# Kernel tuning notes

Hardware: AMD Instinct MI355X
Metric: run time of the kernel (lower is better)

Reference implementation:

```python
import jax, jax.numpy as jnp
import numpy as np

BLOCK_SIZE = 8
SELECT_TOPK = 32
HIDDEN = 512
CHANNELS = 384
NUM_HEADS = 8
B, H, W = 8, 64, 64


def setup_inputs() -> dict:
    key = jax.random.key(0)
    ks = jax.random.split(key, 8)
    num_block_tot = (H // BLOCK_SIZE) * (W // BLOCK_SIZE)
    bs2 = BLOCK_SIZE * BLOCK_SIZE
    x = jax.random.normal(ks[0], (B, H, W, CHANNELS), dtype=jnp.float32)
    aw = jax.random.normal(ks[1], (NUM_HEADS, B, num_block_tot, bs2, bs2 + SELECT_TOPK), dtype=jnp.float32)
    attn_weights = jax.nn.softmax(aw, axis=-1)  # module expects sum(-1)==1
    weights = jax.random.uniform(ks[2], (B, num_block_tot, SELECT_TOPK), dtype=jnp.float32)
    indexes = jax.random.randint(ks[3], (B, num_block_tot, SELECT_TOPK), 0, H * W)
    in_proj_w = jax.random.normal(ks[4], (3 * HIDDEN, CHANNELS), dtype=jnp.float32) * 0.02
    in_proj_b = jax.random.normal(ks[5], (3 * HIDDEN,), dtype=jnp.float32) * 0.02
    out_proj_w = jax.random.normal(ks[6], (CHANNELS, HIDDEN), dtype=jnp.float32) * 0.02
    out_proj_b = jax.random.normal(ks[7], (CHANNELS,), dtype=jnp.float32) * 0.02
    return {"x": x, "attn_weights": attn_weights, "weights": weights,
            "in_proj_w": in_proj_w, "in_proj_b": in_proj_b,
            "out_proj_w": out_proj_w, "out_proj_b": out_proj_b,
            "indexes": indexes}


def reference(x, attn_weights, weights, in_proj_w, in_proj_b, out_proj_w, out_proj_b, indexes):
    batch, height, width, _ = x.shape
    bsz = BLOCK_SIZE
    nbh, nbw = height // bsz, width // bsz
    nbt = nbh * nbw
    num_heads = attn_weights.shape[0]
    hid = HIDDEN
    hd = hid // num_heads
    topk = SELECT_TOPK

    proj = jnp.einsum('bhwc,oc->bhwo', x, in_proj_w) + in_proj_b  # (B,H,W,3*hid)
    s, xh, y = jnp.split(proj, 3, axis=-1)
    xh = xh * jnp.tanh(s)  # Balancer/Whiten/Identity are identity in fwd

    # top-k gathered tokens: (B, nbt, topk, hid) without (B,nbt,num_tokens,hid) blowup
    x_flat = xh.reshape(batch, height * width, hid)
    sel = jax.vmap(lambda xf, ix: xf[ix])(x_flat, indexes)  # (B,nbt,topk,hid)
    sel = sel * weights[..., None]
    sel = sel.reshape(batch, nbt, topk, num_heads, hd).transpose(3, 0, 1, 2, 4)  # (nh,B,nbt,topk,hd)

    # block-local tokens: (nh, B, nbt, bsz^2, hd)
    blk = xh.reshape(batch, nbh, bsz, nbw, bsz, num_heads, hd)
    blk = blk.transpose(5, 0, 1, 3, 2, 4, 6).reshape(num_heads, batch, nbt, bsz * bsz, hd)

    kv = jnp.concatenate([blk, sel], axis=3)  # (nh,B,nbt,bsz^2+topk,hd)
    out = jnp.einsum('hbnqk,hbnkd->hbnqd', attn_weights, kv)  # (nh,B,nbt,bsz^2,hd)

    out = out.reshape(num_heads, batch, nbh, nbw, bsz, bsz, hd)
    out = out.transpose(1, 2, 4, 3, 5, 0, 6).reshape(batch, height, width, hid)
    out = out * y
    return jnp.einsum('bhwd,cd->bhwc', out, out_proj_w) + out_proj_b
```

## Files before the change

### kernel.cpp

```cpp
#include <hip/hip_runtime.h>
#include <hip/hip_bf16.h>
#include <stdint.h>

#define CH   384
#define HID  512
#define NHD  8
#define MTOT 32768

typedef __attribute__((ext_vector_type(8))) short bf16x8;
typedef __attribute__((ext_vector_type(4))) float f32x4;
typedef unsigned short u16;

__device__ __forceinline__ float bf2f(u16 v){ return __uint_as_float(((unsigned)v)<<16); }
__device__ __forceinline__ u16 f2bf(float f){
  unsigned u = __float_as_uint(f);
  return (u16)((u + 0x7fffu + ((u>>16)&1u)) >> 16);
}
__device__ __forceinline__ void gload_lds16(const void* g, void* l){
  __builtin_amdgcn_global_load_lds((const __attribute__((address_space(1))) void*)g,
                                   (__attribute__((address_space(3))) void*)l, 16, 0, 0);
}

__global__ void k_cvt(const float* __restrict__ in, u16* __restrict__ out, int n4){
  int i = blockIdx.x*blockDim.x + threadIdx.x;
  int stride = gridDim.x*blockDim.x;
  for (; i < n4; i += stride){
    float4 v = ((const float4*)in)[i];
    ushort4 o; o.x=f2bf(v.x); o.y=f2bf(v.y); o.z=f2bf(v.z); o.w=f2bf(v.w);
    ((ushort4*)out)[i] = o;
  }
}

__global__ void k_gemm1(const u16* __restrict__ xb, const u16* __restrict__ w1b,
                        const float* __restrict__ b1,
                        u16* __restrict__ xh, u16* __restrict__ yb)
{
  __shared__ short lA[128*64];
  __shared__ short lB[96*64];
  const int tid = threadIdx.x;
  const int w = tid >> 6, lw = tid & 63;
  const int m0 = blockIdx.x * 128;
  const int h0 = blockIdx.y * 32;

  f32x4 acc[2][6] = {};

  for (int kt = 0; kt < CH/64; ++kt){
    const int kbase = kt*64;
    #pragma unroll
    for (int i = 0; i < 4; ++i){
      int chunk = i*4 + w;
      int row = chunk*8 + (lw>>3);
      int sl  = (lw&7) ^ (row&7);
      gload_lds16(xb + (size_t)(m0+row)*CH + kbase + sl*8, &lA[chunk*512]);
    }
    #pragma unroll
    for (int i = 0; i < 3; ++i){
      int chunk = i*4 + w;
      int row = chunk*8 + (lw>>3);
      int grow = (row>>5)*HID + h0 + (row&31);
      int sl = (lw&7) ^ (row&7);
      gload_lds16(w1b + (size_t)grow*CH + kbase + sl*8, &lB[chunk*512]);
    }
    __syncthreads();
    #pragma unroll
    for (int ks = 0; ks < 2; ++ks){
      bf16x8 af[2], bfr[6];
      #pragma unroll
      for (int mi=0; mi<2; ++mi){
        int row = w*32 + mi*16 + (lw&15);
        int sl = (ks*4 + (lw>>4)) ^ (row&7);
        af[mi] = *(const bf16x8*)&lA[row*64 + sl*8];
      }
      #pragma unroll
      for (int nj=0; nj<6; ++nj){
        int row = nj*16 + (lw&15);
        int sl = (ks*4 + (lw>>4)) ^ (row&7);
        bfr[nj] = *(const bf16x8*)&lB[row*64 + sl*8];
      }
      #pragma unroll
      for (int mi=0; mi<2; ++mi)
        #pragma unroll
        for (int nj=0; nj<6; ++nj)
          acc[mi][nj] = __builtin_amdgcn_mfma_f32_16x16x32_bf16(af[mi], bfr[nj], acc[mi][nj], 0,0,0);
    }
    __syncthreads();
  }

  const int lc = lw & 15, lr4 = (lw>>4)*4;
  #pragma unroll
  for (int f=0; f<2; ++f){
    int col = h0 + f*16 + lc;
    float bs = b1[col], bx = b1[512+col], by = b1[1024+col];
    #pragma unroll
    for (int mi=0; mi<2; ++mi){
      #pragma unroll
      for (int j=0; j<4; ++j){
        int row = m0 + w*32 + mi*16 + lr4 + j;
        float s  = acc[mi][0+f][j] + bs;
        float xv = (acc[mi][2+f][j] + bx) * tanhf(s);
        float yv = acc[mi][4+f][j] + by;
        xh[(size_t)row*HID + col] = f2bf(xv);
        yb[(size_t)row*HID + col] = f2bf(yv);
      }
    }
  }
}

__global__ void k_attn(const float* __restrict__ aw, const float* __restrict__ wts,
                       const int* __restrict__ idxs,
                       const u16* __restrict__ xh, const u16* __restrict__ yb,
                       u16* __restrict__ zb)
{
  __shared__ short lAt[64*120];
  __shared__ short lKv[64*96];
  const int tid = threadIdx.x;
  const int bid = blockIdx.x;
  const int h = bid >> 9;
  const int b = (bid >> 6) & 7;
  const int n = bid & 63;
  const int bh = n >> 3, bw = n & 7;

  {
    const float4* src = (const float4*)(aw + (size_t)bid * (64*96));
    #pragma unroll
    for (int i=0; i<24; ++i){
      int f4 = i*64 + tid;
      int q = f4/24, c = f4 - q*24;
      float4 v = src[f4];
      ushort4 o; o.x=f2bf(v.x); o.y=f2bf(v.y); o.z=f2bf(v.z); o.w=f2bf(v.w);
      *(ushort4*)&lAt[q*120 + c*4] = o;
    }
  }
  {
    const int dg = tid & 7;
    #pragma unroll
    for (int it=0; it<12; ++it){
      int t = it*8 + (tid>>3);
      size_t srow; float scale;
      if (t < 64){
        int pix = (bh*8 + (t>>3))*64 + bw*8 + (t&7);
        srow = (size_t)b*4096 + pix; scale = 1.f;
      } else {
        int e = (b*64+n)*32 + (t-64);
        srow = (size_t)b*4096 + idxs[e];
        scale = wts[e];
      }
      bf16x8 v = *(const bf16x8*)&xh[srow*HID + h*64 + dg*8];
      #pragma unroll
      for (int j2=0; j2<8; ++j2){
        int d = dg*8 + j2;
        float f = bf2f((u16)v[j2]) * scale;
        lKv[(d*96 + t) ^ (dg<<3)] = (short)f2bf(f);
      }
    }
  }
  __syncthreads();

  f32x4 acc[4][4] = {};
  const int lc = tid & 15, lk = tid >> 4;
  #pragma unroll
  for (int ks=0; ks<3; ++ks){
    bf16x8 af[4], bv[4];
    #pragma unroll
    for (int mi=0; mi<4; ++mi)
      af[mi] = *(const bf16x8*)&lAt[(mi*16+lc)*120 + ks*32 + lk*8];
    #pragma unroll
    for (int nj=0; nj<4; ++nj){
      int d = nj*16 + lc;
      int idx = (d*96 + ks*32 + lk*8) ^ ((d>>3)<<3);
      bv[nj] = *(const bf16x8*)&lKv[idx];
    }
    #pragma unroll
    for (int mi=0; mi<4; ++mi)
      #pragma unroll
      for (int nj=0; nj<4; ++nj)
        acc[mi][nj] = __builtin_amdgcn_mfma_f32_16x16x32_bf16(af[mi], bv[nj], acc[mi][nj], 0,0,0);
  }

  #pragma unroll
  for (int mi=0; mi<4; ++mi){
    #pragma unroll
    for (int nj=0; nj<4; ++nj){
      int d = nj*16 + lc;
      size_t gcol = (size_t)h*64 + d;
      #pragma unroll
      for (int j=0; j<4; ++j){
        int q = mi*16 + lk*4 + j;
        int pix = (bh*8 + (q>>3))*64 + bw*8 + (q&7);
        size_t r = (size_t)b*4096 + pix;
        float yv = bf2f(yb[r*HID + gcol]);
        zb[r*HID + gcol] = f2bf(acc[mi][nj][j] * yv);
      }
    }
  }
}

__global__ void k_gemm2(const u16* __restrict__ zb, const u16* __restrict__ w2b,
                        const float* __restrict__ b2, float* __restrict__ out)
{
  __shared__ short lA[128*64];
  __shared__ short lB[128*64];
  const int tid = threadIdx.x;
  const int w = tid>>6, lw = tid&63;
  const int wm = w>>1, wn = w&1;
  const int m0 = blockIdx.x*128, n0 = blockIdx.y*128;

  f32x4 acc[4][4] = {};

  for (int kt=0; kt<HID/64; ++kt){
    int kbase = kt*64;
    #pragma unroll
    for (int i=0; i<4; ++i){
      int chunk = i*4 + w;
      int row = chunk*8 + (lw>>3);
      int sl = (lw&7) ^ (row&7);
      gload_lds16(zb  + (size_t)(m0+row)*HID + kbase + sl*8, &lA[chunk*512]);
      gload_lds16(w2b + (size_t)(n0+row)*HID + kbase + sl*8, &lB[chunk*512]);
    }
    __syncthreads();
    #pragma unroll
    for (int ks=0; ks<2; ++ks){
      bf16x8 af[4], bb[4];
      #pragma unroll
      for (int mi=0; mi<4; ++mi){
        int row = wm*64 + mi*16 + (lw&15);
        int sl = (ks*4 + (lw>>4)) ^ (row&7);
        af[mi] = *(const bf16x8*)&lA[row*64 + sl*8];
      }
      #pragma unroll
      for (int nj=0; nj<4; ++nj){
        int row = wn*64 + nj*16 + (lw&15);
        int sl = (ks*4 + (lw>>4)) ^ (row&7);
        bb[nj] = *(const bf16x8*)&lB[row*64 + sl*8];
      }
      #pragma unroll
      for (int mi=0; mi<4; ++mi)
        #pragma unroll
        for (int nj=0; nj<4; ++nj)
          acc[mi][nj] = __builtin_amdgcn_mfma_f32_16x16x32_bf16(af[mi], bb[nj], acc[mi][nj], 0,0,0);
    }
    __syncthreads();
  }

  const int lc = lw&15, lr4 = (lw>>4)*4;
  #pragma unroll
  for (int nj=0; nj<4; ++nj){
    int col = n0 + wn*64 + nj*16 + lc;
    float bias = b2[col];
    #pragma unroll
    for (int mi=0; mi<4; ++mi){
      #pragma unroll
      for (int j=0; j<4; ++j){
        int row = m0 + wm*64 + mi*16 + lr4 + j;
        out[(size_t)row*CH + col] = acc[mi][nj][j] + bias;
      }
    }
  }
}

extern "C" void kernel_launch(void* const* d_in, const int* in_sizes, int n_in,
                              void* d_out, int out_size, void* d_ws, size_t ws_size,
                              hipStream_t stream) {
  const float* x   = (const float*)d_in[0];
  const float* aw  = (const float*)d_in[1];
  const float* wts = (const float*)d_in[2];
  const float* w1  = (const float*)d_in[3];
  const float* b1  = (const float*)d_in[4];
  const float* w2  = (const float*)d_in[5];
  const float* b2  = (const float*)d_in[6];
  const int*   idx = (const int*)d_in[7];
  float* out = (float*)d_out;

  char* ws = (char*)d_ws;
  u16* x_bf  = (u16*)(ws);
  u16* w1_bf = (u16*)(ws + 25165824);
  u16* w2_bf = (u16*)(ws + 26345472);
  u16* xh_bf = (u16*)(ws + 26738688);
  u16* y_bf  = (u16*)(ws + 60293120);
  u16* z_bf  = (u16*)(ws + 93847552);

  k_cvt<<<2048, 256, 0, stream>>>(x,  x_bf,  MTOT*CH/4);
  k_cvt<<<576,  256, 0, stream>>>(w1, w1_bf, 3*HID*CH/4);
  k_cvt<<<192,  256, 0, stream>>>(w2, w2_bf, CH*HID/4);

  k_gemm1<<<dim3(MTOT/128, HID/32), 256, 0, stream>>>(x_bf, w1_bf, b1, xh_bf, y_bf);
  k_attn<<<NHD*8*64, 64, 0, stream>>>(aw, wts, idx, xh_bf, y_bf, z_bf);
  k_gemm2<<<dim3(MTOT/128, CH/128), 256, 0, stream>>>(z_bf, w2_bf, b2, out);
}
```

Baseline: 155.3 us.

## Fold top-k weights into attention matrix and load attention directly to registers

The attention weights are now read from global memory straight into MFMA A-fragments in registers instead of being staged through LDS, and the per-token top-k scale is applied to the attention columns rather than to the gathered K/V rows. The K/V gather packs two tokens per 32-bit LDS store and no longer does per-element scale and bf16 reconversion. Launch bounds are added to steer occupancy. This removes an LDS buffer and its round trip and cuts conversion work, at the cost of more registers and less coalesced global loads for the attention matrix.

Result: faster. 151.1 us (-2.7%).

```diff
diff --git a/kernel.cpp b/kernel.cpp
--- a/kernel.cpp
+++ b/kernel.cpp
@@ -106,12 +106,12 @@
   }
 }
 
-__global__ void k_attn(const float* __restrict__ aw, const float* __restrict__ wts,
-                       const int* __restrict__ idxs,
-                       const u16* __restrict__ xh, const u16* __restrict__ yb,
-                       u16* __restrict__ zb)
+__global__ __launch_bounds__(64, 3)
+void k_attn(const float* __restrict__ aw, const float* __restrict__ wts,
+            const int* __restrict__ idxs,
+            const u16* __restrict__ xh, const u16* __restrict__ yb,
+            u16* __restrict__ zb)
 {
-  __shared__ short lAt[64*120];
   __shared__ short lKv[64*96];
   const int tid = threadIdx.x;
   const int bid = blockIdx.x;
@@ -121,36 +121,55 @@
   const int bh = n >> 3, bw = n & 7;
 
   {
-    const float4* src = (const float4*)(aw + (size_t)bid * (64*96));
-    #pragma unroll
-    for (int i=0; i<24; ++i){
-      int f4 = i*64 + tid;
-      int q = f4/24, c = f4 - q*24;
-      float4 v = src[f4];
-      ushort4 o; o.x=f2bf(v.x); o.y=f2bf(v.y); o.z=f2bf(v.z); o.w=f2bf(v.w);
-      *(ushort4*)&lAt[q*120 + c*4] = o;
-    }
-  }
+    const int dg = tid & 7;
+    const int pr = tid >> 3;
+    #pragma unroll
+    for (int it = 0; it < 6; ++it){
+      int pair = it*8 + pr;
+      int t0 = pair*2;
+      size_t r0, r1;
+      if (t0 < 64){
+        int pix = (bh*8 + (t0>>3))*64 + bw*8 + (t0&7);
+        r0 = (size_t)b*4096 + pix;
+        r1 = r0 + 1;
+      } else {
+        int e = (b*64+n)*32 + (t0-64);
+        r0 = (size_t)b*4096 + idxs[e];
+        r1 = (size_t)b*4096 + idxs[e+1];
+      }
+      bf16x8 v0 = *(const bf16x8*)&xh[r0*HID + h*64 + dg*8];
+      bf16x8 v1 = *(const bf16x8*)&xh[r1*HID + h*64 + dg*8];
+      #pragma unroll
+      for (int j = 0; j < 8; ++j){
+        int d = dg*8 + j;
+        int elem = (d*96 + t0) ^ (dg<<3);
+        unsigned pk = (unsigned)(u16)v0[j] | ((unsigned)(u16)v1[j] << 16);
+        *(unsigned*)&lKv[elem] = pk;
+      }
+    }
+  }
+
+  float wv[8];
   {
-    const int dg = tid & 7;
-    #pragma unroll
-    for (int it=0; it<12; ++it){
-      int t = it*8 + (tid>>3);
-      size_t srow; float scale;
-      if (t < 64){
-        int pix = (bh*8 + (t>>3))*64 + bw*8 + (t&7);
-        srow = (size_t)b*4096 + pix; scale = 1.f;
-      } else {
-        int e = (b*64+n)*32 + (t-64);
-        srow = (size_t)b*4096 + idxs[e];
-        scale = wts[e];
-      }
-      bf16x8 v = *(const bf16x8*)&xh[srow*HID + h*64 + dg*8];
-      #pragma unroll
-      for (int j2=0; j2<8; ++j2){
-        int d = dg*8 + j2;
-        float f = bf2f((u16)v[j2]) * scale;
-        lKv[(d*96 + t) ^ (dg<<3)] = (short)f2bf(f);
+    const float* wp = wts + (size_t)(b*64+n)*32 + (tid>>4)*8;
+    float4 a = *(const float4*)wp, c = *(const float4*)(wp+4);
+    wv[0]=a.x; wv[1]=a.y; wv[2]=a.z; wv[3]=a.w;
+    wv[4]=c.x; wv[5]=c.y; wv[6]=c.z; wv[7]=c.w;
+  }
+  const float* awp = aw + (size_t)bid * (64*96);
+  bf16x8 af[3][4];
+  #pragma unroll
+  for (int ks = 0; ks < 3; ++ks){
+    #pragma unroll
+    for (int mi = 0; mi < 4; ++mi){
+      const float* p = awp + (size_t)(mi*16 + (tid&15))*96 + ks*32 + (tid>>4)*8;
+      float4 f0 = *(const float4*)p;
+      float4 f1 = *(const float4*)(p+4);
+      float t[8] = {f0.x,f0.y,f0.z,f0.w,f1.x,f1.y,f1.z,f1.w};
+      #pragma unroll
+      for (int j = 0; j < 8; ++j){
+        float v = (ks == 2) ? t[j]*wv[j] : t[j];
+        af[ks][mi][j] = (short)f2bf(v);
       }
     }
   }
@@ -159,32 +178,29 @@
   f32x4 acc[4][4] = {};
   const int lc = tid & 15, lk = tid >> 4;
   #pragma unroll
-  for (int ks=0; ks<3; ++ks){
-    bf16x8 af[4], bv[4];
-    #pragma unroll
-    for (int mi=0; mi<4; ++mi)
-      af[mi] = *(const bf16x8*)&lAt[(mi*16+lc)*120 + ks*32 + lk*8];
-    #pragma unroll
-    for (int nj=0; nj<4; ++nj){
+  for (int ks = 0; ks < 3; ++ks){
+    bf16x8 bv[4];
+    #pragma unroll
+    for (int nj = 0; nj < 4; ++nj){
       int d = nj*16 + lc;
       int idx = (d*96 + ks*32 + lk*8) ^ ((d>>3)<<3);
       bv[nj] = *(const bf16x8*)&lKv[idx];
     }
     #pragma unroll
-    for (int mi=0; mi<4; ++mi)
-      #pragma unroll
-      for (int nj=0; nj<4; ++nj)
-        acc[mi][nj] = __builtin_amdgcn_mfma_f32_16x16x32_bf16(af[mi], bv[nj], acc[mi][nj], 0,0,0);
-  }
-
-  #pragma unroll
-  for (int mi=0; mi<4; ++mi){
-    #pragma unroll
-    for (int nj=0; nj<4; ++nj){
+    for (int mi = 0; mi < 4; ++mi)
+      #pragma unroll
+      for (int nj = 0; nj < 4; ++nj)
+        acc[mi][nj] = __builtin_amdgcn_mfma_f32_16x16x32_bf16(af[ks][mi], bv[nj], acc[mi][nj], 0,0,0);
+  }
+
+  #pragma unroll
+  for (int mi = 0; mi < 4; ++mi){
+    #pragma unroll
+    for (int nj = 0; nj < 4; ++nj){
       int d = nj*16 + lc;
       size_t gcol = (size_t)h*64 + d;
       #pragma unroll
-      for (int j=0; j<4; ++j){
+      for (int j = 0; j < 4; ++j){
         int q = mi*16 + lk*4 + j;
         int pix = (bh*8 + (q>>3))*64 + bw*8 + (q&7);
         size_t r = (size_t)b*4096 + pix;
```
